# Performance work log

Hardware: AMD Instinct MI355X
Metric: run time of the kernel (lower is better)

The kernel has to match this reference:

```python
import jax, jax.numpy as jnp
import numpy as np
import math

D_MODEL = 1024
N_HEAD = 16
D_K = 64
D_V = 64
EPS = 1e-6


def setup_inputs() -> dict:
    key = jax.random.key(0)
    ks = jax.random.split(key, 10)
    B, S = 4, 2048
    inp = {
        'x_queries': jax.random.normal(ks[0], (B, S, D_MODEL), jnp.float32),
        'x_keys': jax.random.normal(ks[1], (B, S, D_MODEL), jnp.float32),
        'x_values': jax.random.normal(ks[2], (B, S, D_MODEL), jnp.float32),
        'mask': jax.random.randint(ks[3], (B, S, S), 0, 2, jnp.int32),
        # Linear(d_model, n_head*d_k, bias=False) weights stored as [in, out]
        'w_q': jax.random.normal(ks[4], (D_MODEL, N_HEAD * D_K), jnp.float32) * np.sqrt(2.0 / (D_MODEL + D_K)),
        'w_k': jax.random.normal(ks[5], (D_MODEL, N_HEAD * D_K), jnp.float32) * np.sqrt(2.0 / (D_MODEL + D_K)),
        'w_v': jax.random.normal(ks[6], (D_MODEL, N_HEAD * D_V), jnp.float32) * np.sqrt(2.0 / (D_MODEL + D_V)),
        'w_0': jax.random.normal(ks[7], (N_HEAD * D_V, D_MODEL), jnp.float32) * np.sqrt(2.0 / (N_HEAD * D_V + D_MODEL)),
        'gamma': jnp.ones((D_MODEL,), jnp.float32),
        'beta': jnp.zeros((D_MODEL,), jnp.float32),
    }
    return inp


def _layer_norm(x, gamma, beta, eps=EPS):
    # Matches the torch module: std with Bessel correction, eps added to std.
    mean = jnp.mean(x, axis=-1, keepdims=True)
    std = jnp.std(x, axis=-1, keepdims=True, ddof=1)
    return gamma * (x - mean) / (std + eps) + beta


def reference(x_queries, x_keys, x_values, mask, w_q, w_k, w_v, w_0, gamma, beta):
    B, Lq, _ = x_queries.shape
    residual = x_queries
    # Projections -> [B, L, H, D]
    Q = (x_queries @ w_q).reshape(B, Lq, N_HEAD, D_K)
    K = (x_keys @ w_k).reshape(B, x_keys.shape[1], N_HEAD, D_K)
    V = (x_values @ w_v).reshape(B, x_values.shape[1], N_HEAD, D_V)
    # Scaled dot-product attention (scores materialized as in the original bmm path)
    scores = jnp.einsum('bqhd,bkhd->bhqk', Q, K) / math.sqrt(D_K)
    # NOTE: original masked_fill uses eps (not -inf) where mask == 0
    scores = jnp.where(mask[:, None, :, :] == 0, EPS, scores)
    attn = jax.nn.softmax(scores, axis=-1)
    out = jnp.einsum('bhqk,bkhd->bqhd', attn, V).reshape(B, Lq, N_HEAD * D_V)
    out = out @ w_0
    return _layer_norm(out + residual, gamma, beta)
```

## Files before the change

### kernel.cpp

```cpp
#include <hip/hip_runtime.h>
#include <hip/hip_bf16.h>
#include <math.h>

#define DM 1024
#define NH 16
#define DK 64
#define BB 4
#define SS 2048
#define EPSV 1e-6f
#define NE ((size_t)BB * SS * DM)
#define MM ((size_t)DM * DM)
#define QSCALE 0.18033688011112042f

typedef __attribute__((ext_vector_type(8))) short short8;
typedef __attribute__((ext_vector_type(4))) float f32x4;

__device__ inline unsigned short f2bf(float x) {
  unsigned int u = __builtin_bit_cast(unsigned int, x);
  u += 0x7FFF + ((u >> 16) & 1);
  return (unsigned short)(u >> 16);
}
__device__ inline ushort4 f2bf4(float4 v) {
  ushort4 r;
  r.x = f2bf(v.x); r.y = f2bf(v.y); r.z = f2bf(v.z); r.w = f2bf(v.w);
  return r;
}

__device__ inline float fexp2(float x) {
#if __has_builtin(__builtin_amdgcn_exp2f)
  return __builtin_amdgcn_exp2f(x);
#else
  return exp2f(x);
#endif
}

__device__ inline unsigned cvtpk_bf16(float a, float b) {
  unsigned r;
  asm("v_cvt_pk_bf16_f32 %0, %1, %2" : "=v"(r) : "v"(a), "v"(b));
  return r;
}

__device__ inline void gl_lds16(const unsigned short* g, unsigned short* l) {
  __builtin_amdgcn_global_load_lds((const __attribute__((address_space(1))) void*)g,
                                   (__attribute__((address_space(3))) void*)l, 16, 0, 0);
}

__global__ __launch_bounds__(256) void cvt_x_k(const float* __restrict__ xq,
                                               const float* __restrict__ xk,
                                               const float* __restrict__ xv,
                                               unsigned short* __restrict__ oq,
                                               unsigned short* __restrict__ ok,
                                               unsigned short* __restrict__ ov) {
  const size_t NF4 = NE / 4;
  size_t g = (size_t)blockIdx.x * 256 + threadIdx.x;
  int t = (int)(g / NF4);
  size_t i = g - (size_t)t * NF4;
  const float* s = (t == 0) ? xq : (t == 1) ? xk : xv;
  unsigned short* d = (t == 0) ? oq : (t == 1) ? ok : ov;
  float4 v = ((const float4*)s)[i];
  ((ushort4*)d)[i] = f2bf4(v);
}

__global__ __launch_bounds__(256) void cvt_wT_k(const float* __restrict__ w0,
                                                const float* __restrict__ w1,
                                                const float* __restrict__ w2,
                                                const float* __restrict__ w3,
                                                unsigned short* __restrict__ o0,
                                                unsigned short* __restrict__ o1,
                                                unsigned short* __restrict__ o2,
                                                unsigned short* __restrict__ o3) {
  __shared__ float t[32][33];
  int z = blockIdx.z;
  const float* w = (z == 0) ? w0 : (z == 1) ? w1 : (z == 2) ? w2 : w3;
  unsigned short* o = (z == 0) ? o0 : (z == 1) ? o1 : (z == 2) ? o2 : o3;
  float sc = (z == 0) ? QSCALE : 1.0f;
  int n0 = blockIdx.x * 32, k0 = blockIdx.y * 32;
  int tx = threadIdx.x & 31, ty = threadIdx.x >> 5;
#pragma unroll
  for (int s = 0; s < 4; ++s) t[ty + s * 8][tx] = w[(size_t)(k0 + ty + s * 8) * DM + n0 + tx];
  __syncthreads();
#pragma unroll
  for (int s = 0; s < 4; ++s)
    o[(size_t)(n0 + ty + s * 8) * DM + k0 + tx] = f2bf(t[tx][ty + s * 8] * sc);
}

__global__ __launch_bounds__(256) void maskbits_k(const int* __restrict__ mask,
                                                  unsigned long long* __restrict__ bm) {
  const int total = BB * SS * (SS / 64);
  int lane = threadIdx.x & 63;
  int wid = (blockIdx.x * 256 + threadIdx.x) >> 6;
  int nw = (gridDim.x * 256) >> 6;
  for (int w = wid; w < total; w += nw) {
    int v = mask[(size_t)w * 64 + lane];
    unsigned long long bal = __ballot(v != 0);
    if (lane == 0) bm[w] = bal;
  }
}

template <bool BF16OUT>
__global__ __launch_bounds__(256) void gemm_lds_k(const unsigned short* __restrict__ Abase,
                                                  const unsigned short* __restrict__ WTbase,
                                                  void* __restrict__ Cv, int M, int N, int K,
                                                  size_t zA, size_t zW, size_t zC) {
  __shared__ __align__(16) unsigned short As[128 * 32];
  __shared__ __align__(16) unsigned short Bs[128 * 32];
  const unsigned short* A = Abase + (size_t)blockIdx.z * zA;
  const unsigned short* WT = WTbase + (size_t)blockIdx.z * zW;
  int bm = blockIdx.y * 128, bn = blockIdx.x * 128;
  int tid = threadIdx.x, lane = tid & 63, w = tid >> 6;
  int quad = lane >> 4, c = lane & 15, wx = w & 1, wy = w >> 1;

  f32x4 acc[4][4];
#pragma unroll
  for (int mt = 0; mt < 4; ++mt)
#pragma unroll
    for (int nt = 0; nt < 4; ++nt)
#pragma unroll
      for (int r = 0; r < 4; ++r) acc[mt][nt][r] = 0.f;

  int srow = lane >> 2, scol = (lane & 3) * 8;
  const unsigned short* Ag = A + (size_t)(bm + w * 32 + srow) * K + scol;
  const unsigned short* Bg = WT + (size_t)(bn + w * 32 + srow) * K + scol;
  unsigned short* Al = &As[w * 32 * 32];
  unsigned short* Bl = &Bs[w * 32 * 32];

  for (int k0 = 0; k0 < K; k0 += 32) {
    gl_lds16(Ag + k0, Al);
    gl_lds16(Ag + (size_t)16 * K + k0, Al + 16 * 32);
    gl_lds16(Bg + k0, Bl);
    gl_lds16(Bg + (size_t)16 * K + k0, Bl + 16 * 32);
    __syncthreads();
    short8 af[4], bf[4];
#pragma unroll
    for (int mt = 0; mt < 4; ++mt) af[mt] = *(const short8*)&As[(wy * 64 + mt * 16 + c) * 32 + quad * 8];
#pragma unroll
    for (int nt = 0; nt < 4; ++nt) bf[nt] = *(const short8*)&Bs[(wx * 64 + nt * 16 + c) * 32 + quad * 8];
#pragma unroll
    for (int mt = 0; mt < 4; ++mt)
#pragma unroll
      for (int nt = 0; nt < 4; ++nt)
        acc[mt][nt] = __builtin_amdgcn_mfma_f32_16x16x32_bf16(af[mt], bf[nt], acc[mt][nt], 0, 0, 0);
    __syncthreads();
  }
#pragma unroll
  for (int mt = 0; mt < 4; ++mt)
#pragma unroll
    for (int nt = 0; nt < 4; ++nt)
#pragma unroll
      for (int r = 0; r < 4; ++r) {
        size_t idx = (size_t)blockIdx.z * zC +
                     (size_t)(bm + wy * 64 + mt * 16 + quad * 4 + r) * N + bn + wx * 64 + nt * 16 + c;
        if (BF16OUT)
          ((unsigned short*)Cv)[idx] = f2bf(acc[mt][nt][r]);
        else
          ((float*)Cv)[idx] = acc[mt][nt][r];
      }
}

__global__ __launch_bounds__(256) void attn_mfma_k(const unsigned short* __restrict__ Q,
                                                   const unsigned short* __restrict__ Kg,
                                                   const unsigned short* __restrict__ V,
                                                   const unsigned long long* __restrict__ bm,
                                                   unsigned short* __restrict__ O) {
  __shared__ __align__(16) unsigned short Ks[64 * 64];
  __shared__ __align__(16) unsigned short VB[64 * 64];
  int b = blockIdx.z, h = blockIdx.y, q0 = blockIdx.x * 64;
  int tid = threadIdx.x, lane = tid & 63, w = tid >> 6;
  int quad = lane >> 4, c = lane & 15;

  short8 qf[2];
  {
    const unsigned short* qp = Q + ((size_t)b * SS + q0 + w * 16 + c) * DM + h * DK + quad * 8;
    qf[0] = *(const short8*)qp;
    qf[1] = *(const short8*)(qp + 32);
  }
  const unsigned long long* bp = bm + ((size_t)b * SS + q0 + w * 16 + c) * (SS / 64);
  const int shq = quad * 4;

  short8 ones8;
#pragma unroll
  for (int j = 0; j < 8; ++j) ones8[j] = (short)0x3F80;

  f32x4 accO[4], lacc;
#pragma unroll
  for (int r = 0; r < 4; ++r) lacc[r] = 0.f;
#pragma unroll
  for (int dt = 0; dt < 4; ++dt)
#pragma unroll
    for (int r = 0; r < 4; ++r) accO[dt][r] = 0.f;

  int kr = tid >> 3;
  int kcc = (tid & 7) ^ (kr & 7);
  const unsigned short* pK0 = Kg + ((size_t)b * SS + kr) * DM + h * DK + kcc * 8;
  const unsigned short* pK1 = pK0 + (size_t)32 * DM;
  unsigned short* KlA = &Ks[w * 512];
  unsigned short* KlB = &Ks[2048 + w * 512];

  int vcp = tid & 7, vjh = (tid >> 3) & 1, vdt = (tid >> 4) & 3;
  const unsigned short* pVg =
      V + ((size_t)b * SS + 16 * vjh + 4 * w) * DM + h * DK + 16 * vdt + 2 * vcp;
  unsigned short* vw0 = &VB[(4 * vdt + w) * 128 + 16 * vcp + 4 * vjh];

  const unsigned short* kf0 = &Ks[c * 64 + ((quad ^ (c & 7)) * 8)];
  const unsigned short* kf1 = &Ks[c * 64 + (((4 + quad) ^ (c & 7)) * 8)];

  for (int kt = 0; kt < SS / 64; ++kt) {
    gl_lds16(pK0, KlA);
    gl_lds16(pK1, KlB);
    pK0 += (size_t)64 * DM; pK1 += (size_t)64 * DM;
#pragma unroll
    for (int s = 0; s < 2; ++s) {
      const unsigned short* vp = pVg + (size_t)(32 * s) * DM;
      unsigned L0 = *(const unsigned*)vp;
      unsigned L1 = *(const unsigned*)(vp + DM);
      unsigned L2 = *(const unsigned*)(vp + 2 * (size_t)DM);
      unsigned L3 = *(const unsigned*)(vp + 3 * (size_t)DM);
      ushort4 lo4, hi4;
      lo4.x = (unsigned short)L0; lo4.y = (unsigned short)L1;
      lo4.z = (unsigned short)L2; lo4.w = (unsigned short)L3;
      hi4.x = (unsigned short)(L0 >> 16); hi4.y = (unsigned short)(L1 >> 16);
      hi4.z = (unsigned short)(L2 >> 16); hi4.w = (unsigned short)(L3 >> 16);
      *(ushort4*)(vw0 + s * 2048) = lo4;
      *(ushort4*)(vw0 + s * 2048 + 8) = hi4;
    }
    pVg += (size_t)64 * DM;
    __syncthreads();

    f32x4 sacc[4];
#pragma unroll
    for (int nt = 0; nt < 4; ++nt) {
#pragma unroll
      for (int r = 0; r < 4; ++r) sacc[nt][r] = 0.f;
      short8 ka = *(const short8*)(kf0 + nt * 1024);
      short8 kb = *(const short8*)(kf1 + nt * 1024);
      sacc[nt] = __builtin_amdgcn_mfma_f32_16x16x32_bf16(ka, qf[0], sacc[nt], 0, 0, 0);
      sacc[nt] = __builtin_amdgcn_mfma_f32_16x16x32_bf16(kb, qf[1], sacc[nt], 0, 0, 0);
    }

    unsigned long long msh = bp[kt] >> shq;
    unsigned mlo = (unsigned)msh, mhi = (unsigned)(msh >> 32);
    unsigned padw[8];
#pragma unroll
    for (int nt = 0; nt < 4; ++nt) {
      unsigned msel = (nt & 2) ? mhi : mlo;
      const int bse = (nt & 1) * 16;
      float pv[4];
#pragma unroll
      for (int r = 0; r < 4; ++r) {
        float ex = fexp2(sacc[nt][r]);
        pv[r] = ((msel >> (bse + r)) & 1u) ? ex : 1.0f;
      }
      padw[nt * 2] = cvtpk_bf16(pv[0], pv[1]);
      padw[nt * 2 + 1] = cvtpk_bf16(pv[2], pv[3]);
    }

#pragma unroll
    for (int pkt = 0; pkt < 2; ++pkt) {
      union { unsigned u[4]; short8 s8; } pa;
#pragma unroll
      for (int i = 0; i < 4; ++i) pa.u[i] = padw[pkt * 4 + i];
      lacc = __builtin_amdgcn_mfma_f32_16x16x32_bf16(pa.s8, ones8, lacc, 0, 0, 0);
#pragma unroll
      for (int dt = 0; dt < 4; ++dt) {
        short8 vf = *(const short8*)&VB[((pkt * 4 + dt) * 4 + quad) * 128 + c * 8];
        accO[dt] = __builtin_amdgcn_mfma_f32_16x16x32_bf16(pa.s8, vf, accO[dt], 0, 0, 0);
      }
    }
    __syncthreads();
  }

  float inv[4];
#pragma unroll
  for (int r = 0; r < 4; ++r) inv[r] = 1.f / lacc[r];
#pragma unroll
  for (int dt = 0; dt < 4; ++dt)
#pragma unroll
    for (int r = 0; r < 4; ++r) {
      int q = q0 + w * 16 + quad * 4 + r;
      O[((size_t)b * SS + q) * DM + h * DK + dt * 16 + c] = f2bf(accO[dt][r] * inv[r]);
    }
}

__global__ __launch_bounds__(256) void ln_k(const float* __restrict__ P,
                                            const float* __restrict__ X,
                                            const float* __restrict__ gamma,
                                            const float* __restrict__ beta,
                                            float* __restrict__ out) {
  __shared__ float sm[4];
  int row = blockIdx.x, tid = threadIdx.x, w = tid >> 6;
  float4 p = ((const float4*)(P + (size_t)row * DM))[tid];
  float4 x = ((const float4*)(X + (size_t)row * DM))[tid];
  float4 v = make_float4(p.x + x.x, p.y + x.y, p.z + x.z, p.w + x.w);
  float s = (v.x + v.y) + (v.z + v.w);
#pragma unroll
  for (int off = 1; off < 64; off <<= 1) s += __shfl_xor(s, off);
  if ((tid & 63) == 0) sm[w] = s;
  __syncthreads();
  float mean = (sm[0] + sm[1] + sm[2] + sm[3]) * (1.f / DM);
  __syncthreads();
  float dx = v.x - mean, dy = v.y - mean, dz = v.z - mean, dw = v.w - mean;
  float s2 = (dx * dx + dy * dy) + (dz * dz + dw * dw);
#pragma unroll
  for (int off = 1; off < 64; off <<= 1) s2 += __shfl_xor(s2, off);
  if ((tid & 63) == 0) sm[w] = s2;
  __syncthreads();
  float var = (sm[0] + sm[1] + sm[2] + sm[3]) * (1.f / (DM - 1));
  float inv = 1.f / (sqrtf(var) + EPSV);
  float4 g = ((const float4*)gamma)[tid];
  float4 be = ((const float4*)beta)[tid];
  float4 y = make_float4(g.x * dx * inv + be.x, g.y * dy * inv + be.y,
                         g.z * dz * inv + be.z, g.w * dw * inv + be.w);
  ((float4*)(out + (size_t)row * DM))[tid] = y;
}

extern "C" void kernel_launch(void* const* d_in, const int* in_sizes, int n_in,
                              void* d_out, int out_size, void* d_ws, size_t ws_size,
                              hipStream_t stream) {
  const float* xq = (const float*)d_in[0];
  const float* xk = (const float*)d_in[1];
  const float* xv = (const float*)d_in[2];
  const int* mask = (const int*)d_in[3];
  const float* wq = (const float*)d_in[4];
  const float* wk = (const float*)d_in[5];
  const float* wv = (const float*)d_in[6];
  const float* w0 = (const float*)d_in[7];
  const float* gamma = (const float*)d_in[8];
  const float* beta = (const float*)d_in[9];
  float* out = (float*)d_out;

  unsigned short* xqb = (unsigned short*)d_ws;
  unsigned short* xkb = xqb + NE;
  unsigned short* xvb = xkb + NE;
  unsigned short* wTq = xvb + NE;
  unsigned short* wTk = wTq + MM;
  unsigned short* wTv = wTk + MM;
  unsigned short* wT0 = wTv + MM;
  unsigned short* Qb = wT0 + MM;
  unsigned short* Kb = Qb + NE;
  unsigned short* Vb = Kb + NE;
  unsigned short* AOb = Vb + NE;
  float* P = (float*)Qb;
  unsigned long long* bm = (unsigned long long*)d_out;

  const int M = BB * SS;
  cvt_x_k<<<(unsigned)(3 * (NE / 4) / 256), 256, 0, stream>>>(xq, xk, xv, xqb, xkb, xvb);
  cvt_wT_k<<<dim3(32, 32, 4), 256, 0, stream>>>(wq, wk, wv, w0, wTq, wTk, wTv, wT0);
  maskbits_k<<<256, 256, 0, stream>>>(mask, bm);
  gemm_lds_k<true><<<dim3(DM / 128, M / 128, 3), 256, 0, stream>>>(
      xqb, wTq, Qb, M, DM, DM, NE, MM, NE);
  attn_mfma_k<<<dim3(SS / 64, NH, BB), 256, 0, stream>>>(Qb, Kb, Vb, bm, AOb);
  gemm_lds_k<false><<<dim3(DM / 128, M / 128, 1), 256, 0, stream>>>(
      AOb, wT0, P, M, DM, DM, 0, 0, 0);
  ln_k<<<M, 256, 0, stream>>>(P, xq, gamma, beta, out);
}
```

Baseline: 550.4 us.

## Pre-transpose V and double-buffer K/V tiles with async LDS loads

Adds a kernel that writes V in a per-head [D, S] layout into a reused workspace buffer, so the attention kernel can fetch V with the same async global-to-LDS 16-byte loads used for K. It replaces the old scalar V gather and in-register transpose. K and V LDS tiles are double-buffered so the next tile's load overlaps the current tile's MFMA work, and one barrier per tile is dropped. The cost is an extra launch plus a full read and write of V, twice the LDS footprint, and a new swizzled V fragment read pattern.

```diff
diff --git a/kernel.cpp b/kernel.cpp
--- a/kernel.cpp
+++ b/kernel.cpp
@@ -13,6 +13,7 @@
 #define QSCALE 0.18033688011112042f
 
 typedef __attribute__((ext_vector_type(8))) short short8;
+typedef __attribute__((ext_vector_type(4))) short short4v;
 typedef __attribute__((ext_vector_type(4))) float f32x4;
 
 __device__ inline unsigned short f2bf(float x) {
@@ -97,6 +98,30 @@
   }
 }
 
+__global__ __launch_bounds__(256) void vtrans_k(const unsigned short* __restrict__ Vb,
+                                                unsigned short* __restrict__ VT) {
+  __shared__ unsigned short t[64][72];
+  int b = blockIdx.z, h = blockIdx.y, s0 = blockIdx.x * 64;
+  int tid = threadIdx.x;
+#pragma unroll
+  for (int p = 0; p < 2; ++p) {
+    int idx = p * 256 + tid;
+    int r = idx >> 3, cch = (idx & 7) * 8;
+    short8 v = *(const short8*)&Vb[((size_t)b * SS + s0 + r) * DM + h * DK + cch];
+    *(short8*)&t[r][cch] = v;
+  }
+  __syncthreads();
+#pragma unroll
+  for (int p = 0; p < 2; ++p) {
+    int idx = p * 256 + tid;
+    int d = idx >> 3, sch = (idx & 7) * 8;
+    union { short8 v; unsigned short u[8]; } pk;
+#pragma unroll
+    for (int j = 0; j < 8; ++j) pk.u[j] = t[sch + j][d];
+    *(short8*)&VT[(((size_t)b * NH + h) * DK + d) * SS + s0 + sch] = pk.v;
+  }
+}
+
 template <bool BF16OUT>
 __global__ __launch_bounds__(256) void gemm_lds_k(const unsigned short* __restrict__ Abase,
                                                   const unsigned short* __restrict__ WTbase,
@@ -159,11 +184,11 @@
 
 __global__ __launch_bounds__(256) void attn_mfma_k(const unsigned short* __restrict__ Q,
                                                    const unsigned short* __restrict__ Kg,
-                                                   const unsigned short* __restrict__ V,
+                                                   const unsigned short* __restrict__ VT,
                                                    const unsigned long long* __restrict__ bm,
                                                    unsigned short* __restrict__ O) {
-  __shared__ __align__(16) unsigned short Ks[64 * 64];
-  __shared__ __align__(16) unsigned short VB[64 * 64];
+  __shared__ __align__(16) unsigned short Ks[2][64 * 64];
+  __shared__ __align__(16) unsigned short Vs[2][64 * 64];
   int b = blockIdx.z, h = blockIdx.y, q0 = blockIdx.x * 64;
   int tid = threadIdx.x, lane = tid & 63, w = tid >> 6;
   int quad = lane >> 4, c = lane & 15;
@@ -190,49 +215,44 @@
     for (int r = 0; r < 4; ++r) accO[dt][r] = 0.f;
 
   int kr = tid >> 3;
-  int kcc = (tid & 7) ^ (kr & 7);
-  const unsigned short* pK0 = Kg + ((size_t)b * SS + kr) * DM + h * DK + kcc * 8;
+  int scc = (tid & 7) ^ (kr & 7);
+  const unsigned short* pK0 = Kg + ((size_t)b * SS + kr) * DM + h * DK + scc * 8;
   const unsigned short* pK1 = pK0 + (size_t)32 * DM;
-  unsigned short* KlA = &Ks[w * 512];
-  unsigned short* KlB = &Ks[2048 + w * 512];
-
-  int vcp = tid & 7, vjh = (tid >> 3) & 1, vdt = (tid >> 4) & 3;
-  const unsigned short* pVg =
-      V + ((size_t)b * SS + 16 * vjh + 4 * w) * DM + h * DK + 16 * vdt + 2 * vcp;
-  unsigned short* vw0 = &VB[(4 * vdt + w) * 128 + 16 * vcp + 4 * vjh];
-
-  const unsigned short* kf0 = &Ks[c * 64 + ((quad ^ (c & 7)) * 8)];
-  const unsigned short* kf1 = &Ks[c * 64 + (((4 + quad) ^ (c & 7)) * 8)];
-
-  for (int kt = 0; kt < SS / 64; ++kt) {
-    gl_lds16(pK0, KlA);
-    gl_lds16(pK1, KlB);
-    pK0 += (size_t)64 * DM; pK1 += (size_t)64 * DM;
-#pragma unroll
-    for (int s = 0; s < 2; ++s) {
-      const unsigned short* vp = pVg + (size_t)(32 * s) * DM;
-      unsigned L0 = *(const unsigned*)vp;
-      unsigned L1 = *(const unsigned*)(vp + DM);
-      unsigned L2 = *(const unsigned*)(vp + 2 * (size_t)DM);
-      unsigned L3 = *(const unsigned*)(vp + 3 * (size_t)DM);
-      ushort4 lo4, hi4;
-      lo4.x = (unsigned short)L0; lo4.y = (unsigned short)L1;
-      lo4.z = (unsigned short)L2; lo4.w = (unsigned short)L3;
-      hi4.x = (unsigned short)(L0 >> 16); hi4.y = (unsigned short)(L1 >> 16);
-      hi4.z = (unsigned short)(L2 >> 16); hi4.w = (unsigned short)(L3 >> 16);
-      *(ushort4*)(vw0 + s * 2048) = lo4;
-      *(ushort4*)(vw0 + s * 2048 + 8) = hi4;
-    }
-    pVg += (size_t)64 * DM;
+  const unsigned short* pV0 = VT + (((size_t)b * NH + h) * DK + kr) * SS + scc * 8;
+  const unsigned short* pV1 = pV0 + (size_t)32 * SS;
+
+  const int kfo0 = c * 64 + ((quad ^ (c & 7)) * 8);
+  const int kfo1 = c * 64 + (((4 + quad) ^ (c & 7)) * 8);
+  const int vfo0 = c * 64 + ((((quad >> 1)) ^ (c & 7)) * 8) + (quad & 1) * 4;
+  const int vfo1 = c * 64 + (((4 + (quad >> 1)) ^ (c & 7)) * 8) + (quad & 1) * 4;
+
+  const int NT = SS / 64;
+
+  gl_lds16(pK0, &Ks[0][w * 512]);
+  gl_lds16(pK1, &Ks[0][2048 + w * 512]);
+  gl_lds16(pV0, &Vs[0][w * 512]);
+  gl_lds16(pV1, &Vs[0][2048 + w * 512]);
+  pK0 += (size_t)64 * DM; pK1 += (size_t)64 * DM;
+  pV0 += 64; pV1 += 64;
+
+  auto tile = [&](int buf, int kt) {
     __syncthreads();
+    if (kt + 1 < NT) {
+      gl_lds16(pK0, &Ks[buf ^ 1][w * 512]);
+      gl_lds16(pK1, &Ks[buf ^ 1][2048 + w * 512]);
+      gl_lds16(pV0, &Vs[buf ^ 1][w * 512]);
+      gl_lds16(pV1, &Vs[buf ^ 1][2048 + w * 512]);
+      pK0 += (size_t)64 * DM; pK1 += (size_t)64 * DM;
+      pV0 += 64; pV1 += 64;
+    }
 
     f32x4 sacc[4];
 #pragma unroll
     for (int nt = 0; nt < 4; ++nt) {
 #pragma unroll
       for (int r = 0; r < 4; ++r) sacc[nt][r] = 0.f;
-      short8 ka = *(const short8*)(kf0 + nt * 1024);
-      short8 kb = *(const short8*)(kf1 + nt * 1024);
+      short8 ka = *(const short8*)&Ks[buf][kfo0 + nt * 1024];
+      short8 kb = *(const short8*)&Ks[buf][kfo1 + nt * 1024];
       sacc[nt] = __builtin_amdgcn_mfma_f32_16x16x32_bf16(ka, qf[0], sacc[nt], 0, 0, 0);
       sacc[nt] = __builtin_amdgcn_mfma_f32_16x16x32_bf16(kb, qf[1], sacc[nt], 0, 0, 0);
     }
@@ -260,13 +280,21 @@
 #pragma unroll
       for (int i = 0; i < 4; ++i) pa.u[i] = padw[pkt * 4 + i];
       lacc = __builtin_amdgcn_mfma_f32_16x16x32_bf16(pa.s8, ones8, lacc, 0, 0, 0);
+      const int vfo = pkt ? vfo1 : vfo0;
 #pragma unroll
       for (int dt = 0; dt < 4; ++dt) {
-        short8 vf = *(const short8*)&VB[((pkt * 4 + dt) * 4 + quad) * 128 + c * 8];
-        accO[dt] = __builtin_amdgcn_mfma_f32_16x16x32_bf16(pa.s8, vf, accO[dt], 0, 0, 0);
+        int e1 = vfo + dt * 1024;
+        union { short4v h[2]; short8 s8; } vf;
+        vf.h[0] = *(const short4v*)&Vs[buf][e1];
+        vf.h[1] = *(const short4v*)&Vs[buf][e1 ^ 16];
+        accO[dt] = __builtin_amdgcn_mfma_f32_16x16x32_bf16(pa.s8, vf.s8, accO[dt], 0, 0, 0);
       }
     }
-    __syncthreads();
+  };
+
+  for (int kt2 = 0; kt2 < NT; kt2 += 2) {
+    tile(0, kt2);
+    tile(1, kt2 + 1);
   }
 
   float inv[4];
@@ -339,6 +367,7 @@
   unsigned short* Kb = Qb + NE;
   unsigned short* Vb = Kb + NE;
   unsigned short* AOb = Vb + NE;
+  unsigned short* VTb = xvb;
   float* P = (float*)Qb;
   unsigned long long* bm = (unsigned long long*)d_out;
 
@@ -348,7 +377,8 @@
   maskbits_k<<<256, 256, 0, stream>>>(mask, bm);
   gemm_lds_k<true><<<dim3(DM / 128, M / 128, 3), 256, 0, stream>>>(
       xqb, wTq, Qb, M, DM, DM, NE, MM, NE);
-  attn_mfma_k<<<dim3(SS / 64, NH, BB), 256, 0, stream>>>(Qb, Kb, Vb, bm, AOb);
+  vtrans_k<<<dim3(SS / 64, NH, BB), 256, 0, stream>>>(Vb, VTb);
+  attn_mfma_k<<<dim3(SS / 64, NH, BB), 256, 0, stream>>>(Qb, Kb, VTb, bm, AOb);
   gemm_lds_k<false><<<dim3(DM / 128, M / 128, 1), 256, 0, stream>>>(
       AOb, wT0, P, M, DM, DM, 0, 0, 0);
   ln_k<<<M, 256, 0, stream>>>(P, xq, gamma, beta, out);
```

New measurement: 549.2 us. No clear change (-0.2%).
